# Kernel tuning notes

Hardware: AMD Instinct MI355X
Metric: run time of the kernel (lower is better)

Reference implementation:

```python
import jax, jax.numpy as jnp
import numpy as np

N_NODES = 50000
N_EDGES = 800000
IN_CH = 64
OUT_CH = 64
HEADS = 4
NEG_SLOPE = 0.2  # PyG GATConv default


def setup_inputs() -> dict:
    key = jax.random.key(0)
    ks = jax.random.split(key, 8)
    x = jax.random.normal(ks[0], (N_NODES, IN_CH), dtype=jnp.float32)
    edge_index = jax.random.randint(ks[1], (2, N_EDGES), 0, N_NODES, dtype=jnp.int64)
    # GATConv params (concat=False): lin weight [in, H*out], att vectors [H, out], bias [out]
    W = jax.random.normal(ks[2], (IN_CH, HEADS * OUT_CH), dtype=jnp.float32) * (1.0 / np.sqrt(IN_CH))
    att_src = jax.random.normal(ks[3], (HEADS, OUT_CH), dtype=jnp.float32) * 0.1
    att_dst = jax.random.normal(ks[4], (HEADS, OUT_CH), dtype=jnp.float32) * 0.1
    bias = jnp.zeros((OUT_CH,), dtype=jnp.float32)
    fc_w = jax.random.normal(ks[5], (OUT_CH, 1), dtype=jnp.float32) * (1.0 / np.sqrt(OUT_CH))
    fc_b = jnp.zeros((1,), dtype=jnp.float32)
    return {"x": x, "edge_index": edge_index, "W": W, "att_src": att_src,
            "att_dst": att_dst, "bias": bias, "fc_w": fc_w, "fc_b": fc_b}


def reference(x, edge_index, W, att_src, att_dst, bias, fc_w, fc_b):
    N = x.shape[0]
    H, C = att_src.shape
    # per-node linear transform -> [N, H, C]
    xt = (x @ W).reshape(N, H, C)
    # PyG default add_self_loops=True
    loop = jnp.arange(N, dtype=edge_index.dtype)
    src = jnp.concatenate([edge_index[0], loop])  # message source j
    dst = jnp.concatenate([edge_index[1], loop])  # aggregation target i
    # attention logits: a_l . x_j + a_r . x_i, leaky_relu
    a_src = jnp.einsum('nhc,hc->nh', xt, att_src)  # [N, H]
    a_dst = jnp.einsum('nhc,hc->nh', xt, att_dst)
    e = jax.nn.leaky_relu(a_src[src] + a_dst[dst], NEG_SLOPE)  # [E, H]
    # segment softmax over incoming edges of each dst node
    m = jax.ops.segment_max(e, dst, num_segments=N)            # [N, H]
    e = jnp.exp(e - m[dst])
    s = jax.ops.segment_sum(e, dst, num_segments=N)            # [N, H]
    alpha = e / s[dst]                                          # [E, H]
    # weighted scatter-aggregate
    msg = xt[src] * alpha[:, :, None]                           # [E, H, C]
    out = jax.ops.segment_sum(msg, dst, num_segments=N)         # [N, H, C]
    out = out.mean(axis=1) + bias                               # concat=False -> mean heads
    h = jax.nn.relu(out)
    scores = (h @ fc_w + fc_b).squeeze(-1)                      # [N]
    return scores
```

## Files before the change

kernel.cpp:

```cpp
#include <hip/hip_runtime.h>
#include <hip/hip_bf16.h>

#define N_NODES 50000
#define N_EDGES 800000
#define HEADS   4
#define NEG_SLOPE 0.2f
#define CAP     64
#define NT      ((N_NODES + 63) / 64)
#define EPB     2048
#define NEB     ((N_EDGES + EPB - 1) / EPB)
#define NREG    98
#define QCAP    9216
#define INV_LN2 1.44269504088896340736f

typedef __attribute__((ext_vector_type(8))) _Float16 half8;
typedef __attribute__((ext_vector_type(4))) float f32x4;
typedef __attribute__((ext_vector_type(8))) unsigned short u16x8;

template <typename T> __device__ __forceinline__ float cvt(T v);
template <> __device__ __forceinline__ float cvt<float>(float v) { return v; }
template <> __device__ __forceinline__ float cvt<__hip_bfloat16>(__hip_bfloat16 v) {
    return __bfloat162float(v);
}
__device__ __forceinline__ unsigned short f2h(float f) {
    _Float16 h = (_Float16)f;
    return __builtin_bit_cast(unsigned short, h);
}
__device__ __forceinline__ float hbits(unsigned short u) {
    return (float)__builtin_bit_cast(_Float16, u);
}
__device__ __forceinline__ int probe_fp32(const unsigned* xw) {
    int sane = 0;
    for (int j = 0; j < 64; ++j) {
        unsigned e = (xw[j] >> 7) & 0xFF;
        sane += (e >= 90 && e <= 141);
    }
    return sane < 32;
}
__device__ __forceinline__ float loadW(int isf32, const void* W, int idx) {
    return isf32 ? ((const float*)W)[idx]
                 : cvt<__hip_bfloat16>(((const __hip_bfloat16*)W)[idx]);
}

template <typename T>
__device__ __forceinline__ void load8_f16(const T* p, _Float16* dst);
template <>
__device__ __forceinline__ void load8_f16<float>(const float* p, _Float16* dst) {
    float4 a = *(const float4*)p;
    float4 b = *(const float4*)(p + 4);
    dst[0] = (_Float16)a.x; dst[1] = (_Float16)a.y;
    dst[2] = (_Float16)a.z; dst[3] = (_Float16)a.w;
    dst[4] = (_Float16)b.x; dst[5] = (_Float16)b.y;
    dst[6] = (_Float16)b.z; dst[7] = (_Float16)b.w;
}
template <>
__device__ __forceinline__ void load8_f16<__hip_bfloat16>(const __hip_bfloat16* p,
                                                          _Float16* dst) {
    uint4 a = *(const uint4*)p;
    const unsigned short* u = (const unsigned short*)&a;
#pragma unroll
    for (int j = 0; j < 8; ++j)
        dst[j] = (_Float16)__uint_as_float(((unsigned)u[j]) << 16);
}

__global__ __launch_bounds__(256) void k_init(const unsigned* __restrict__ xw,
                                              const int* __restrict__ ei,
                                              const void* __restrict__ W,
                                              const void* __restrict__ att_src,
                                              const void* __restrict__ att_dst,
                                              int* __restrict__ qcnt,
                                              int* __restrict__ flags,
                                              unsigned short* __restrict__ Batt,
                                              unsigned short* __restrict__ Bpost) {
    __shared__ float waS[256], waD[256];
    __shared__ int f32sh;
    if (blockIdx.x == 0) {
        if (threadIdx.x < NREG) qcnt[threadIdx.x] = 0;
        if (threadIdx.x == 0) {
            int all0 = 1;
            for (int j = 1; j < 64; j += 2) all0 &= (ei[j] == 0);
            flags[0] = all0;
            flags[1] = probe_fp32(xw);
        }
        return;
    }
    const int pb = blockIdx.x - 1;
    if (threadIdx.x == 0) f32sh = probe_fp32(xw);
    __syncthreads();
    const int isf32 = f32sh;
    if (pb == 0) {
        int t = threadIdx.x, k = t >> 2, h = t & 3;
        float s = 0.f, d = 0.f;
        for (int c = 0; c < 64; ++c) {
            float w = loadW(isf32, W, k * 256 + h * 64 + c);
            float as = isf32 ? ((const float*)att_src)[h * 64 + c]
                             : cvt<__hip_bfloat16>(((const __hip_bfloat16*)att_src)[h * 64 + c]);
            float ad = isf32 ? ((const float*)att_dst)[h * 64 + c]
                             : cvt<__hip_bfloat16>(((const __hip_bfloat16*)att_dst)[h * 64 + c]);
            s = fmaf(w, as, s);
            d = fmaf(w, ad, d);
        }
        waS[t] = s * INV_LN2;
        waD[t] = d * INV_LN2;
        __syncthreads();
        if (threadIdx.x < 128) {
            int r = threadIdx.x;
            int q = (r >> 6) & 1, l = r & 63, n = l & 15;
            int kbase = q * 32 + ((l >> 4) & 3) * 8;
#pragma unroll
            for (int j = 0; j < 8; ++j) {
                int kk = kbase + j;
                float v = (n < 4) ? waS[kk * 4 + n]
                        : (n < 8) ? waD[kk * 4 + (n - 4)] : 0.f;
                Batt[r * 8 + j] = f2h(v);
            }
        }
    } else {
        const int sub = threadIdx.x >> 5, s = threadIdx.x & 31;
        const int t = (pb - 1) * 8 + sub;
        const int kt = t >> 2, nt = t & 3;
#pragma unroll
        for (int e = 0; e < 16; ++e) {
            int idx = s * 16 + e;
            int l = idx >> 3, j = idx & 7;
            int rs = kt * 32 + ((l >> 4) & 3) * 8 + j;
            int h = rs >> 6, k_in = rs & 63;
            int c = nt * 16 + (l & 15);
            Bpost[t * 512 + l * 8 + j] =
                f2h(loadW(isf32, W, k_in * 256 + h * 64 + c) * 0.25f);
        }
    }
}

template <typename T>
__device__ __forceinline__ void row_body(const T* __restrict__ x,
                                         const unsigned short* __restrict__ Batt,
                                         unsigned short* __restrict__ x16,
                                         float* __restrict__ a_src,
                                         float* __restrict__ a_dst) {
    const int tid = threadIdx.x;
    const int wav = tid >> 6, lane = tid & 63;
    const int quad = lane >> 4, r15 = lane & 15;
    const int m0 = blockIdx.x * 64;
    int gr = m0 + wav * 16 + r15;
    if (gr >= N_NODES) gr = N_NODES - 1;
    half8 afrag[2];
#pragma unroll
    for (int q = 0; q < 2; ++q) {
        _Float16 tmp[8];
        load8_f16<T>(x + (size_t)gr * 64 + q * 32 + quad * 8, tmp);
#pragma unroll
        for (int j = 0; j < 8; ++j) afrag[q][j] = tmp[j];
    }
    f32x4 acc = (f32x4){0.f, 0.f, 0.f, 0.f};
    const half8* bp = (const half8*)Batt;
    acc = __builtin_amdgcn_mfma_f32_16x16x32_f16(afrag[0], bp[lane], acc, 0, 0, 0);
    acc = __builtin_amdgcn_mfma_f32_16x16x32_f16(afrag[1], bp[64 + lane], acc, 0, 0, 0);
    if (r15 < 8) {
#pragma unroll
        for (int r = 0; r < 4; ++r) {
            int grow = m0 + wav * 16 + quad * 4 + r;
            if (grow < N_NODES) {
                if (r15 < 4) a_src[grow * HEADS + r15]       = acc[r];
                else         a_dst[grow * HEADS + (r15 - 4)] = acc[r];
            }
        }
    }
    {
        int row = m0 + (tid >> 2), seg = tid & 3;
        if (row < N_NODES) {
            _Float16 tmp[16];
            load8_f16<T>(x + (size_t)row * 64 + seg * 16, tmp);
            load8_f16<T>(x + (size_t)row * 64 + seg * 16 + 8, tmp + 8);
            *(u16x8*)(x16 + (size_t)row * 64 + seg * 16)     = *(const u16x8*)tmp;
            *(u16x8*)(x16 + (size_t)row * 64 + seg * 16 + 8) = *(const u16x8*)(tmp + 8);
        }
    }
}

__global__ __launch_bounds__(256) void k_mid(const void* __restrict__ x,
                                             const unsigned short* __restrict__ Batt,
                                             const int* __restrict__ ei,
                                             const int* __restrict__ flags,
                                             int* __restrict__ qcnt,
                                             unsigned* __restrict__ queue,
                                             unsigned short* __restrict__ x16,
                                             float* __restrict__ a_src,
                                             float* __restrict__ a_dst) {
    __shared__ int hist[NREG];
    __shared__ int qbaseS[NREG];
    const int tid = threadIdx.x;
    const bool edge_blk = ((blockIdx.x & 1) == 0);
    const int eb = blockIdx.x >> 1;
    unsigned rec[8]; int reg[8], lpos[8];
    int histv = 0, mybase = 0;
    if (edge_blk) {
        if (tid < NREG) hist[tid] = 0;
        __syncthreads();
        const int f64 = flags[0];
        const int base = eb * EPB + tid;
#pragma unroll
        for (int k = 0; k < 8; ++k) {
            int t = base + k * 256;
            if (t < N_EDGES) {
                int s, d;
                if (f64) { s = ei[2 * t]; d = ei[2 * N_EDGES + 2 * t]; }
                else     { s = ei[t];     d = ei[N_EDGES + t]; }
                reg[k] = d >> 9;
                rec[k] = (unsigned)s | ((unsigned)d << 16);
            } else reg[k] = -1;
        }
#pragma unroll
        for (int k = 0; k < 8; ++k)
            if (reg[k] >= 0) lpos[k] = atomicAdd(&hist[reg[k]], 1);
        __syncthreads();
        if (tid < NREG) {
            histv = hist[tid];
            if (histv) mybase = atomicAdd(qcnt + tid, histv);
        }
    }
    if (flags[1]) row_body<float>((const float*)x, Batt, x16, a_src, a_dst);
    else          row_body<__hip_bfloat16>((const __hip_bfloat16*)x, Batt,
                                           x16, a_src, a_dst);
    if (edge_blk) {
        if (tid < NREG) qbaseS[tid] = mybase;
        __syncthreads();
#pragma unroll
        for (int k = 0; k < 8; ++k)
            if (reg[k] >= 0) {
                int o = qbaseS[reg[k]] + lpos[k];
                if (o < QCAP)
                    queue[(size_t)reg[k] * QCAP + o] = rec[k];
            }
    }
}

__global__ __launch_bounds__(256) void k_scat(const unsigned* __restrict__ queue,
                                              const int* __restrict__ qcnt,
                                              unsigned short* __restrict__ col_pad,
                                              int* __restrict__ cnt) {
    __shared__ int cl[512];
    const int b = blockIdx.x, tid = threadIdx.x;
    const int base = b << 9;
    cl[tid] = 0; cl[tid + 256] = 0;
    __syncthreads();
    int m = qcnt[b]; m = m > QCAP ? QCAP : m;
    const unsigned* q = queue + (size_t)b * QCAP;
#pragma unroll 4
    for (int i = tid; i < m; i += 256) {
        unsigned rec = q[i];
        int d = rec >> 16, s = rec & 0xffff;
        int p = atomicAdd(&cl[d - base], 1);
        if (p < CAP) col_pad[(size_t)d * CAP + p] = (unsigned short)s;
    }
    __syncthreads();
    int j = base + tid;
    if (j < N_NODES) cnt[j] = cl[tid];
    j += 256;
    if (j < N_NODES) cnt[j] = cl[tid + 256];
}

__global__ __launch_bounds__(256) void k_aggregate(const int* __restrict__ cnt,
                                                   const unsigned short* __restrict__ col_pad,
                                                   const float* __restrict__ a_src,
                                                   const float* __restrict__ a_dst,
                                                   const unsigned short* __restrict__ x16,
                                                   unsigned short* __restrict__ s_cat) {
    __shared__ __align__(16) int cS[4][64];
    __shared__ float4 peS[4][64];
    const int tid = threadIdx.x;
    const int wav = tid >> 6, lane = tid & 63;
    const int hlf = lane >> 5, l5 = lane & 31;
    const int wid = (blockIdx.x * blockDim.x + tid) >> 6;
    if (wid >= N_NODES) return;
    int* cSw = cS[wav];
    float4* peSw = peS[wav];
    int n = cnt[wid]; n = n > (CAP - 1) ? (CAP - 1) : n;
    const float4 ad = ((const float4*)a_dst)[wid];
    int mycol = wid;
    if (lane < n) mycol = (int)col_pad[wid * CAP + lane];
    const float4 as = ((const float4*)a_src)[mycol];
    float e0 = as.x + ad.x, e1 = as.y + ad.y;
    float e2 = as.z + ad.z, e3 = as.w + ad.w;
    e0 = e0 > 0.f ? e0 : NEG_SLOPE * e0;  e1 = e1 > 0.f ? e1 : NEG_SLOPE * e1;
    e2 = e2 > 0.f ? e2 : NEG_SLOPE * e2;  e3 = e3 > 0.f ? e3 : NEG_SLOPE * e3;
    float4 pe = make_float4(exp2f(e0), exp2f(e1), exp2f(e2), exp2f(e3));
    if (lane > n) pe = make_float4(0.f, 0.f, 0.f, 0.f);
    const int slot = (lane & 1) * 32 + (lane >> 1);
    cSw[slot] = mycol << 7;
    peS[wav][slot] = pe;
    const char* xb = (const char*)x16 + l5 * 4;
    float a0 = 0.f, a1 = 0.f, a2 = 0.f, a3 = 0.f;
    float a4 = 0.f, a5 = 0.f, a6 = 0.f, a7 = 0.f;
    float sp0 = 0.f, sp1 = 0.f, sp2 = 0.f, sp3 = 0.f;
    const int nr = (n + 2) >> 1;
    const int*    cB = cSw + hlf * 32;
    const float4* pB = peSw + hlf * 32;
#define ACC2(D, P) { float x0 = hbits((unsigned short)((D) & 0xffff)); \
                     float x1 = hbits((unsigned short)((D) >> 16)); \
                     a0 = fmaf((P).x, x0, a0); a1 = fmaf((P).x, x1, a1); \
                     a2 = fmaf((P).y, x0, a2); a3 = fmaf((P).y, x1, a3); \
                     a4 = fmaf((P).z, x0, a4); a5 = fmaf((P).z, x1, a5); \
                     a6 = fmaf((P).w, x0, a6); a7 = fmaf((P).w, x1, a7); \
                     sp0 += (P).x; sp1 += (P).y; sp2 += (P).z; sp3 += (P).w; }
    int r = 0;
    for (; r + 4 <= nr; r += 4) {
        const int4 cc = *(const int4*)(cB + r);
        unsigned dA = *(const unsigned*)(xb + cc.x);
        unsigned dB = *(const unsigned*)(xb + cc.y);
        unsigned dC = *(const unsigned*)(xb + cc.z);
        unsigned dD = *(const unsigned*)(xb + cc.w);
        float4 pA = pB[r], pBv = pB[r + 1], pC = pB[r + 2], pD = pB[r + 3];
        ACC2(dA, pA); ACC2(dB, pBv); ACC2(dC, pC); ACC2(dD, pD);
    }
    for (; r < nr; ++r) {
        int c = cB[r];
        unsigned d = *(const unsigned*)(xb + c);
        float4 p = pB[r];
        ACC2(d, p);
    }
#undef ACC2
    a0 += __shfl_xor(a0, 32, 64); a1 += __shfl_xor(a1, 32, 64);
    a2 += __shfl_xor(a2, 32, 64); a3 += __shfl_xor(a3, 32, 64);
    a4 += __shfl_xor(a4, 32, 64); a5 += __shfl_xor(a5, 32, 64);
    a6 += __shfl_xor(a6, 32, 64); a7 += __shfl_xor(a7, 32, 64);
    sp0 += __shfl_xor(sp0, 32, 64); sp1 += __shfl_xor(sp1, 32, 64);
    sp2 += __shfl_xor(sp2, 32, 64); sp3 += __shfl_xor(sp3, 32, 64);
    const float r0 = 1.f / sp0, r1 = 1.f / sp1;
    const float r2 = 1.f / sp2, r3 = 1.f / sp3;
    unsigned short* sr = s_cat + (size_t)wid * 256 + 2 * l5;
    unsigned w0 = (unsigned)f2h(a0 * r0) | ((unsigned)f2h(a1 * r0) << 16);
    unsigned w1 = (unsigned)f2h(a2 * r1) | ((unsigned)f2h(a3 * r1) << 16);
    unsigned w2 = (unsigned)f2h(a4 * r2) | ((unsigned)f2h(a5 * r2) << 16);
    unsigned w3 = (unsigned)f2h(a6 * r3) | ((unsigned)f2h(a7 * r3) << 16);
    *(unsigned*)(sr)       = w0;
    *(unsigned*)(sr + 64)  = w1;
    *(unsigned*)(sr + 128) = w2;
    *(unsigned*)(sr + 192) = w3;
}

template <typename T>
__device__ __forceinline__ void post_body(const unsigned short* __restrict__ s_cat,
                                          const unsigned short* __restrict__ Bpost,
                                          const T* __restrict__ bias,
                                          const T* __restrict__ fc_w,
                                          const T* __restrict__ fc_b,
                                          float* __restrict__ out) {
    const int tid = threadIdx.x;
    const int wav = tid >> 6, lane = tid & 63;
    const int quad = lane >> 4, r15 = lane & 15;
    const int m0 = blockIdx.x * 64;
    int gr = m0 + wav * 16 + r15;
    if (gr >= N_NODES) gr = N_NODES - 1;
    const half8* arow = (const half8*)((const char*)s_cat + (size_t)gr * 512);
    half8 af[8];
#pragma unroll
    for (int kt = 0; kt < 8; ++kt) af[kt] = arow[kt * 4 + quad];
    f32x4 acc[4];
#pragma unroll
    for (int nt = 0; nt < 4; ++nt) acc[nt] = (f32x4){0.f, 0.f, 0.f, 0.f};
    const half8* bp = (const half8*)Bpost;
#pragma unroll
    for (int kt = 0; kt < 8; ++kt)
#pragma unroll
        for (int nt = 0; nt < 4; ++nt)
            acc[nt] = __builtin_amdgcn_mfma_f32_16x16x32_f16(
                af[kt], bp[(kt * 4 + nt) * 64 + lane], acc[nt], 0, 0, 0);
    float bi[4], fw[4];
#pragma unroll
    for (int nt = 0; nt < 4; ++nt) {
        int c = nt * 16 + r15;
        bi[nt] = cvt<T>(bias[c]);
        fw[nt] = cvt<T>(fc_w[c]);
    }
    const float fcb = cvt<T>(fc_b[0]);
#pragma unroll
    for (int r = 0; r < 4; ++r) {
        float p = 0.f;
#pragma unroll
        for (int nt = 0; nt < 4; ++nt) {
            float o = acc[nt][r] + bi[nt];
            o = o > 0.f ? o : 0.f;
            p = fmaf(o, fw[nt], p);
        }
#pragma unroll
        for (int off = 8; off > 0; off >>= 1) p += __shfl_xor(p, off, 64);
        int row = m0 + wav * 16 + quad * 4 + r;
        if (r15 == 0 && row < N_NODES) out[row] = p + fcb;
    }
}

__global__ __launch_bounds__(256) void k_post(const unsigned short* __restrict__ s_cat,
                                              const unsigned short* __restrict__ Bpost,
                                              const void* __restrict__ bias,
                                              const void* __restrict__ fc_w,
                                              const void* __restrict__ fc_b,
                                              const int* __restrict__ flags,
                                              float* __restrict__ out) {
    if (flags[1])
        post_body<float>(s_cat, Bpost, (const float*)bias, (const float*)fc_w,
                         (const float*)fc_b, out);
    else
        post_body<__hip_bfloat16>(s_cat, Bpost, (const __hip_bfloat16*)bias,
                                  (const __hip_bfloat16*)fc_w,
                                  (const __hip_bfloat16*)fc_b, out);
}

extern "C" void kernel_launch(void* const* d_in, const int* in_sizes, int n_in,
                              void* d_out, int out_size, void* d_ws, size_t ws_size,
                              hipStream_t stream) {
    const void* x       = d_in[0];
    const int*  ei      = (const int*)d_in[1];
    const void* W       = d_in[2];
    const void* att_src = d_in[3];
    const void* att_dst = d_in[4];
    const void* bias    = d_in[5];
    const void* fc_w    = d_in[6];
    const void* fc_b    = d_in[7];
    float* out = (float*)d_out;

    char* wsb = (char*)d_ws;
    unsigned short* x16   = (unsigned short*)wsb;
    unsigned short* s_cat = (unsigned short*)(wsb + 6400000);
    unsigned* queue = (unsigned*)s_cat;
    unsigned short* Batt  = (unsigned short*)(wsb + 32000000);
    unsigned short* Bpost = (unsigned short*)(wsb + 32002048);
    float* a_src = (float*)(wsb + 32034816);
    float* a_dst = (float*)(wsb + 32834816);
    unsigned short* col_pad = (unsigned short*)(wsb + 33634816);
    int* cnt   = (int*)(wsb + 40034816);
    int* flags = (int*)(wsb + 40234816);
    int* qcnt  = (int*)(wsb + 40234824);

    k_init<<<6, 256, 0, stream>>>((const unsigned*)x, ei, W, att_src,
                                  att_dst, qcnt, flags, Batt, Bpost);
    k_mid<<<NT, 256, 0, stream>>>(x, Batt, ei, flags, qcnt, queue,
                                  x16, a_src, a_dst);
    k_scat<<<NREG, 256, 0, stream>>>(queue, qcnt, col_pad, cnt);
    k_aggregate<<<((size_t)N_NODES * 64 + 255) / 256, 256, 0, stream>>>(
        cnt, col_pad, a_src, a_dst, x16, s_cat);
    k_post<<<NT, 256, 0, stream>>>(s_cat, Bpost, bias, fc_w, fc_b, flags, out);
}
```

Measured before the change: 174.4 us.

## Halve scatter regions, vectorize edge loads, store neighbor count inside padded row

Doubles the number of destination regions (256 nodes each, half the queue capacity per region), so k_scat runs on 196 blocks instead of 98. Edge indices are now read two per thread with vector loads. The per-node count is stored in the last slot of each padded adjacency row, which removes the separate cnt array and lets k_aggregate get the count from the same row load through a wave shuffle. In exchange, each row holds one fewer neighbor slot, and the smaller queue capacity per region raises the risk of overflow on skewed graphs.

```diff
diff --git a/kernel.cpp b/kernel.cpp
--- a/kernel.cpp
+++ b/kernel.cpp
@@ -8,9 +8,8 @@
 #define CAP     64
 #define NT      ((N_NODES + 63) / 64)
 #define EPB     2048
-#define NEB     ((N_EDGES + EPB - 1) / EPB)
-#define NREG    98
-#define QCAP    9216
+#define NREG    196
+#define QCAP    4608
 #define INV_LN2 1.44269504088896340736f
 
 typedef __attribute__((ext_vector_type(8))) _Float16 half8;
@@ -198,17 +197,27 @@
         if (tid < NREG) hist[tid] = 0;
         __syncthreads();
         const int f64 = flags[0];
-        const int base = eb * EPB + tid;
-#pragma unroll
-        for (int k = 0; k < 8; ++k) {
-            int t = base + k * 256;
-            if (t < N_EDGES) {
-                int s, d;
-                if (f64) { s = ei[2 * t]; d = ei[2 * N_EDGES + 2 * t]; }
-                else     { s = ei[t];     d = ei[N_EDGES + t]; }
-                reg[k] = d >> 9;
-                rec[k] = (unsigned)s | ((unsigned)d << 16);
-            } else reg[k] = -1;
+        const int pbase = eb * 1024 + tid;
+#pragma unroll
+        for (int k = 0; k < 4; ++k) {
+            int pid = pbase + k * 256;
+            int e = 2 * pid;
+            if (e < N_EDGES) {
+                int s0, d0, s1, d1;
+                if (f64) {
+                    int4 sv = *(const int4*)(ei + 2 * e);
+                    int4 dv = *(const int4*)(ei + 2 * N_EDGES + 2 * e);
+                    s0 = sv.x; s1 = sv.z; d0 = dv.x; d1 = dv.z;
+                } else {
+                    int2 sv = *(const int2*)(ei + e);
+                    int2 dv = *(const int2*)(ei + N_EDGES + e);
+                    s0 = sv.x; s1 = sv.y; d0 = dv.x; d1 = dv.y;
+                }
+                reg[2 * k]     = d0 >> 8;
+                rec[2 * k]     = (unsigned)s0 | ((unsigned)d0 << 16);
+                reg[2 * k + 1] = d1 >> 8;
+                rec[2 * k + 1] = (unsigned)s1 | ((unsigned)d1 << 16);
+            } else { reg[2 * k] = -1; reg[2 * k + 1] = -1; }
         }
 #pragma unroll
         for (int k = 0; k < 8; ++k)
@@ -237,31 +246,29 @@
 
 __global__ __launch_bounds__(256) void k_scat(const unsigned* __restrict__ queue,
                                               const int* __restrict__ qcnt,
-                                              unsigned short* __restrict__ col_pad,
-                                              int* __restrict__ cnt) {
-    __shared__ int cl[512];
+                                              unsigned short* __restrict__ col_pad) {
+    __shared__ int cl[256];
     const int b = blockIdx.x, tid = threadIdx.x;
-    const int base = b << 9;
-    cl[tid] = 0; cl[tid + 256] = 0;
+    const int base = b << 8;
+    cl[tid] = 0;
     __syncthreads();
     int m = qcnt[b]; m = m > QCAP ? QCAP : m;
     const unsigned* q = queue + (size_t)b * QCAP;
-#pragma unroll 4
     for (int i = tid; i < m; i += 256) {
         unsigned rec = q[i];
         int d = rec >> 16, s = rec & 0xffff;
         int p = atomicAdd(&cl[d - base], 1);
-        if (p < CAP) col_pad[(size_t)d * CAP + p] = (unsigned short)s;
+        if (p < CAP - 1) col_pad[(size_t)d * CAP + p] = (unsigned short)s;
     }
     __syncthreads();
     int j = base + tid;
-    if (j < N_NODES) cnt[j] = cl[tid];
-    j += 256;
-    if (j < N_NODES) cnt[j] = cl[tid + 256];
-}
-
-__global__ __launch_bounds__(256) void k_aggregate(const int* __restrict__ cnt,
-                                                   const unsigned short* __restrict__ col_pad,
+    if (j < N_NODES) {
+        int c = cl[tid]; c = c > CAP - 1 ? CAP - 1 : c;
+        col_pad[(size_t)j * CAP + (CAP - 1)] = (unsigned short)c;
+    }
+}
+
+__global__ __launch_bounds__(256) void k_aggregate(const unsigned short* __restrict__ col_pad,
                                                    const float* __restrict__ a_src,
                                                    const float* __restrict__ a_dst,
                                                    const unsigned short* __restrict__ x16,
@@ -275,10 +282,10 @@
     if (wid >= N_NODES) return;
     int* cSw = cS[wav];
     float4* peSw = peS[wav];
-    int n = cnt[wid]; n = n > (CAP - 1) ? (CAP - 1) : n;
+    const int cval = (int)col_pad[(size_t)wid * CAP + lane];
+    const int n = __shfl(cval, 63, 64);
     const float4 ad = ((const float4*)a_dst)[wid];
-    int mycol = wid;
-    if (lane < n) mycol = (int)col_pad[wid * CAP + lane];
+    const int mycol = (lane < n) ? cval : wid;
     const float4 as = ((const float4*)a_src)[mycol];
     float e0 = as.x + ad.x, e1 = as.y + ad.y;
     float e2 = as.z + ad.z, e3 = as.w + ad.w;
@@ -428,16 +435,15 @@
     float* a_src = (float*)(wsb + 32034816);
     float* a_dst = (float*)(wsb + 32834816);
     unsigned short* col_pad = (unsigned short*)(wsb + 33634816);
-    int* cnt   = (int*)(wsb + 40034816);
-    int* flags = (int*)(wsb + 40234816);
-    int* qcnt  = (int*)(wsb + 40234824);
+    int* flags = (int*)(wsb + 40034816);
+    int* qcnt  = (int*)(wsb + 40034824);
 
     k_init<<<6, 256, 0, stream>>>((const unsigned*)x, ei, W, att_src,
                                   att_dst, qcnt, flags, Batt, Bpost);
     k_mid<<<NT, 256, 0, stream>>>(x, Batt, ei, flags, qcnt, queue,
                                   x16, a_src, a_dst);
-    k_scat<<<NREG, 256, 0, stream>>>(queue, qcnt, col_pad, cnt);
+    k_scat<<<NREG, 256, 0, stream>>>(queue, qcnt, col_pad);
     k_aggregate<<<((size_t)N_NODES * 64 + 255) / 256, 256, 0, stream>>>(
-        cnt, col_pad, a_src, a_dst, x16, s_cat);
+        col_pad, a_src, a_dst, x16, s_cat);
     k_post<<<NT, 256, 0, stream>>>(s_cat, Bpost, bias, fc_w, fc_b, flags, out);
 }
```

Measured after the change: 165.9 us. -4.9%, faster.
